# Optimization experiments

Hardware: AMD Instinct MI355X
Metric: run time of the kernel (lower is better)

## Reference

```python
import jax, jax.numpy as jnp
import numpy as np

V, D, H, HID, L, C, R, ALPHA = 32000, 768, 12, 3072, 2, 2, 8, 16
B, S = 64, 512
HD = D // H
SCALE = ALPHA / R

def _lin(x, W, b, A, Bm):
    # LoRA linear (eval mode, dropout=identity): x @ W^T + b + scaling * (x @ A^T) @ B^T
    return x @ W.T + b + (x @ A.T) @ Bm.T * SCALE

def _ln(x, g, b):
    m = x.mean(-1, keepdims=True)
    v = ((x - m) ** 2).mean(-1, keepdims=True)
    return (x - m) / jnp.sqrt(v + 1e-5) * g + b

def setup_inputs():
    ks = iter(jax.random.split(jax.random.key(0), 64))
    def nrm(shape):
        return jax.random.normal(next(ks), shape, dtype=jnp.float32) * 0.02
    inp = {"tokens": jax.random.randint(next(ks), (B, S), 0, V)}
    inp["emb_W"] = nrm((V, D)); inp["emb_A"] = nrm((R, V)); inp["emb_B"] = nrm((D, R))
    dims = {"q": (D, D), "k": (D, D), "v": (D, D), "o": (D, D), "1": (D, HID), "2": (HID, D)}
    for nm, (di, do) in dims.items():
        inp["W" + nm] = nrm((L, do, di)); inp["b" + nm] = jnp.zeros((L, do), jnp.float32)
        inp["A" + nm] = nrm((L, R, di)); inp["B" + nm] = nrm((L, do, R))
    inp["g1"] = jnp.ones((L, D), jnp.float32); inp["be1"] = jnp.zeros((L, D), jnp.float32)
    inp["g2"] = jnp.ones((L, D), jnp.float32); inp["be2"] = jnp.zeros((L, D), jnp.float32)
    inp["fcW"] = nrm((C, D)); inp["fcb"] = jnp.zeros((C,), jnp.float32)
    inp["fcA"] = nrm((R, D)); inp["fcB"] = nrm((C, R))
    return inp

def reference(tokens, emb_W, emb_A, emb_B,
              Wq, bq, Aq, Bq, Wk, bk, Ak, Bk, Wv, bv, Av, Bv, Wo, bo, Ao, Bo,
              W1, b1, A1, B1, W2, b2, A2, B2,
              g1, be1, g2, be2, fcW, fcb, fcA, fcB):
    # LoRA embedding: W[tok] + scaling * A^T[tok] @ B^T
    x = emb_W[tokens] + (emb_A.T[tokens] @ emb_B.T) * SCALE      # (B, S, D)
    x = jnp.transpose(x, (1, 0, 2))                              # (S, B, D)
    for l in range(L):
        Q = _lin(x, Wq[l], bq[l], Aq[l], Bq[l]).reshape(S, B, H, HD).transpose(0, 2, 1, 3)
        K = _lin(x, Wk[l], bk[l], Ak[l], Bk[l]).reshape(S, B, H, HD).transpose(0, 2, 1, 3)
        Vt = _lin(x, Wv[l], bv[l], Av[l], Bv[l]).reshape(S, B, H, HD).transpose(0, 2, 1, 3)
        # Faithful to the source: attention mixes over the BATCH axis (S, H, B, B)
        scores = jnp.einsum('shbd,shcd->shbc', Q, K) / jnp.sqrt(jnp.float32(HD))
        probs = jax.nn.softmax(scores, axis=-1)
        ao = jnp.einsum('shbc,shcd->shbd', probs, Vt).transpose(0, 2, 1, 3).reshape(S, B, D)
        ao = _lin(ao, Wo[l], bo[l], Ao[l], Bo[l])
        x = _ln(x + ao, g1[l], be1[l])
        ff = _lin(jax.nn.relu(_lin(x, W1[l], b1[l], A1[l], B1[l])), W2[l], b2[l], A2[l], B2[l])
        x = _ln(x + ff, g2[l], be2[l])
    return _lin(x.mean(0), fcW, fcb, fcA, fcB)                   # (B, C)
```

## Files before the change

kernel.cpp:

```cpp
#include <hip/hip_runtime.h>
#include <hip/hip_bf16.h>

#define VSZ   32000
#define DSZ   768
#define HN    12
#define HIDSZ 3072
#define NL    2
#define CN    2
#define RR    8
#define SCALEF 2.0f
#define BBATCH 64
#define SSEQ  512
#define HDIM  64
#define NTOK  (BBATCH*SSEQ)
#define QKVM  (3*DSZ)

typedef __attribute__((ext_vector_type(8))) short bf16x8;
typedef __attribute__((ext_vector_type(4))) float floatx4;

__device__ __forceinline__ unsigned short f2bf_raw(float f) {
    __hip_bfloat16 h = __float2bfloat16(f);
    return __builtin_bit_cast(unsigned short, h);
}
__device__ __forceinline__ float bf2f(__hip_bfloat16 h) {
    return __bfloat162float(h);
}

__device__ __forceinline__ void gload16(const void* g, void* l) {
    __builtin_amdgcn_global_load_lds(
        (const __attribute__((address_space(1))) unsigned int*)g,
        (__attribute__((address_space(3))) unsigned int*)l, 16, 0, 0);
}

__global__ __launch_bounds__(256) void embed_kernel(
    const int* __restrict__ tokens, const float* __restrict__ embW,
    const float* __restrict__ embA, const float* __restrict__ embB,
    __hip_bfloat16* __restrict__ xb)
{
    int n = blockIdx.x;
    int s = n / BBATCH, b = n % BBATCH;
    int tok = tokens[b * SSEQ + s];
    __shared__ float a[RR];
    if (threadIdx.x < RR) a[threadIdx.x] = embA[(size_t)threadIdx.x * VSZ + tok];
    __syncthreads();
    for (int d = threadIdx.x; d < DSZ; d += 256) {
        float val = embW[(size_t)tok * DSZ + d];
        float lo = 0.f;
        #pragma unroll
        for (int r = 0; r < RR; ++r) lo += a[r] * embB[d * RR + r];
        xb[(size_t)n * DSZ + d] = __float2bfloat16(val + SCALEF * lo);
    }
}

__global__ __launch_bounds__(256) void weff_kernel(
    const float* __restrict__ W, const float* __restrict__ A,
    const float* __restrict__ Bm, __hip_bfloat16* __restrict__ Weff, int K)
{
    int i = blockIdx.x * 256 + threadIdx.x;
    int o = blockIdx.y;
    float acc = W[(size_t)o * K + i];
    #pragma unroll
    for (int r = 0; r < RR; ++r)
        acc += SCALEF * Bm[o * RR + r] * A[(size_t)r * K + i];
    Weff[(size_t)o * K + i] = __float2bfloat16(acc);
}

__global__ __launch_bounds__(256) void biascat_kernel(
    const float* __restrict__ b0, const float* __restrict__ b1v,
    const float* __restrict__ b2v, float* __restrict__ out)
{
    int t = blockIdx.y * 256 + threadIdx.x;
    const float* src = (blockIdx.x == 0) ? b0 : (blockIdx.x == 1) ? b1v : b2v;
    out[blockIdx.x * DSZ + t] = src[t];
}

#define BM2  256
#define BK2  64
#define ABUF (BM2*BK2)

#define SB0() __builtin_amdgcn_sched_barrier(0)

__device__ __forceinline__ void stage_half(
    const unsigned short* __restrict__ g, unsigned short* l,
    int h, int ld, int k0, int t, int sk)
{
    #pragma unroll
    for (int it = 0; it < 2; ++it) {
        int rl = it * 64 + (t >> 3);
        gload16(g + (size_t)(h * 128 + rl) * ld + k0 + sk,
                l + (size_t)(h * 1024 + it * 512 + t) * 8);
    }
}

__device__ __forceinline__ void ph_exit() {
    __builtin_amdgcn_s_setprio(0);
    SB0();
    __builtin_amdgcn_s_barrier();
    SB0();
}

template<bool RELU, bool ADDRES>
__global__ __launch_bounds__(512, 2) void mgemm256_kernel(
    const __hip_bfloat16* __restrict__ X, const __hip_bfloat16* __restrict__ W,
    const float* __restrict__ bias, const __hip_bfloat16* __restrict__ res,
    __hip_bfloat16* __restrict__ Y, int K, int ldx, int ldy)
{
    __shared__ __align__(16) unsigned short As[2 * ABUF];
    __shared__ __align__(16) unsigned short Bs[2 * ABUF];

    const int t    = threadIdx.x;
    const int wv   = t >> 6;
    const int lane = t & 63;
    const int fm   = lane & 15;
    const int fq   = lane >> 4;
    const int wm   = wv >> 2;
    const int wn   = wv & 3;

    const int nbx = gridDim.x;
    const int nby = gridDim.y;
    int lin = blockIdx.y * nbx + blockIdx.x;
    {
        const int nwg = nbx * nby;
        int q = nwg >> 3, r = nwg & 7;
        int xcd = lin & 7, idx = lin >> 3;
        lin = (xcd < r ? xcd * (q + 1) : r * (q + 1) + (xcd - r) * q) + idx;
    }
    const int bn = lin % nby;
    const int bm = lin / nby;

    const unsigned short* Xg = (const unsigned short*)X + (size_t)bm * 256 * ldx;
    const unsigned short* Wg = (const unsigned short*)W + (size_t)bn * 256 * K;
    const int sk = ((t & 7) ^ ((t >> 3) & 7)) * 8;
    const int nt = K / BK2;

    floatx4 acc[2][2][4][2];
    #pragma unroll
    for (int a = 0; a < 2; ++a)
        #pragma unroll
        for (int b = 0; b < 2; ++b)
            #pragma unroll
            for (int c = 0; c < 4; ++c)
                #pragma unroll
                for (int d = 0; d < 2; ++d)
                    acc[a][b][c][d] = (floatx4){0.f, 0.f, 0.f, 0.f};

    const int swzg = (fq ^ (fm & 7)) * 8;
    int aoff[4], boff[2];
    #pragma unroll
    for (int mf = 0; mf < 4; ++mf) aoff[mf] = (wm * 64 + mf * 16 + fm) * 64 + swzg;
    #pragma unroll
    for (int nf = 0; nf < 2; ++nf) boff[nf] = (wn * 32 + nf * 16 + fm) * 64 + swzg;

    stage_half(Xg, As, 0, ldx, 0, t, sk);
    stage_half(Wg, Bs, 0, K,   0, t, sk);
    stage_half(Xg, As, 1, ldx, 0, t, sk);
    stage_half(Wg, Bs, 1, K,   0, t, sk);
    if (nt > 1) {
        stage_half(Xg, As + ABUF, 0, ldx, BK2, t, sk);
        stage_half(Wg, Bs + ABUF, 0, K,   BK2, t, sk);
        stage_half(Wg, Bs + ABUF, 1, K,   BK2, t, sk);
        asm volatile("s_waitcnt vmcnt(6)" ::: "memory");
    } else {
        asm volatile("s_waitcnt vmcnt(0)" ::: "memory");
    }
    SB0();
    __builtin_amdgcn_s_barrier();
    SB0();

    bf16x8 af0[4][2], af1[4][2], bf0[2][2], bf1[2][2];
    #pragma unroll
    for (int mf = 0; mf < 4; ++mf) {
        af0[mf][0] = *(const bf16x8*)&As[aoff[mf]];
        af0[mf][1] = *(const bf16x8*)&As[aoff[mf] ^ 32];
    }
    #pragma unroll
    for (int nf = 0; nf < 2; ++nf) {
        bf0[nf][0] = *(const bf16x8*)&Bs[boff[nf]];
        bf0[nf][1] = *(const bf16x8*)&Bs[boff[nf] ^ 32];
    }
    SB0();

    for (int kt = 0; kt < nt; ++kt) {
        const unsigned short* Ab = As + (kt & 1) * ABUF;
        const unsigned short* Bb = Bs + (kt & 1) * ABUF;
        unsigned short* AobW = As + ((kt & 1) ^ 1) * ABUF;
        const unsigned short* AobR = AobW;
        const unsigned short* BobR = Bs + ((kt & 1) ^ 1) * ABUF;
        unsigned short* Asame = (unsigned short*)Ab;
        unsigned short* Bsame = (unsigned short*)Bb;
        const int k1 = (kt + 1) * BK2;
        const int k2 = (kt + 2) * BK2;

        #pragma unroll
        for (int nf = 0; nf < 2; ++nf) {
            bf1[nf][0] = *(const bf16x8*)&Bb[(boff[nf] + 8192)];
            bf1[nf][1] = *(const bf16x8*)&Bb[(boff[nf] + 8192) ^ 32];
        }
        SB0();
        if (kt + 1 < nt) stage_half(Xg, AobW, 1, ldx, k1, t, sk);
        SB0();
        __builtin_amdgcn_s_barrier();
        asm volatile("s_waitcnt lgkmcnt(4)" ::: "memory");
        SB0();
        __builtin_amdgcn_s_setprio(1);
        #pragma unroll
        for (int mf = 0; mf < 4; ++mf)
            #pragma unroll
            for (int nf = 0; nf < 2; ++nf) {
                acc[0][0][mf][nf] = __builtin_amdgcn_mfma_f32_16x16x32_bf16(
                    af0[mf][0], bf0[nf][0], acc[0][0][mf][nf], 0, 0, 0);
                acc[0][0][mf][nf] = __builtin_amdgcn_mfma_f32_16x16x32_bf16(
                    af0[mf][1], bf0[nf][1], acc[0][0][mf][nf], 0, 0, 0);
            }
        ph_exit();

        #pragma unroll
        for (int mf = 0; mf < 4; ++mf) {
            af1[mf][0] = *(const bf16x8*)&Ab[(aoff[mf] + 8192)];
            af1[mf][1] = *(const bf16x8*)&Ab[(aoff[mf] + 8192) ^ 32];
        }
        SB0();
        if (kt + 2 < nt) stage_half(Xg, Asame, 0, ldx, k2, t, sk);
        SB0();
        __builtin_amdgcn_s_barrier();
        asm volatile("s_waitcnt lgkmcnt(8)" ::: "memory");
        SB0();
        __builtin_amdgcn_s_setprio(1);
        #pragma unroll
        for (int mf = 0; mf < 4; ++mf)
            #pragma unroll
            for (int nf = 0; nf < 2; ++nf) {
                acc[0][1][mf][nf] = __builtin_amdgcn_mfma_f32_16x16x32_bf16(
                    af0[mf][0], bf1[nf][0], acc[0][1][mf][nf], 0, 0, 0);
                acc[0][1][mf][nf] = __builtin_amdgcn_mfma_f32_16x16x32_bf16(
                    af0[mf][1], bf1[nf][1], acc[0][1][mf][nf], 0, 0, 0);
            }
        ph_exit();

        if (kt + 2 < nt) stage_half(Wg, Bsame, 0, K, k2, t, sk);
        SB0();
        __builtin_amdgcn_s_barrier();
        asm volatile("s_waitcnt lgkmcnt(0)" ::: "memory");
        SB0();
        __builtin_amdgcn_s_setprio(1);
        #pragma unroll
        for (int mf = 0; mf < 4; ++mf)
            #pragma unroll
            for (int nf = 0; nf < 2; ++nf) {
                acc[1][0][mf][nf] = __builtin_amdgcn_mfma_f32_16x16x32_bf16(
                    af1[mf][0], bf0[nf][0], acc[1][0][mf][nf], 0, 0, 0);
                acc[1][0][mf][nf] = __builtin_amdgcn_mfma_f32_16x16x32_bf16(
                    af1[mf][1], bf0[nf][1], acc[1][0][mf][nf], 0, 0, 0);
            }
        ph_exit();

        asm volatile("s_waitcnt vmcnt(4)" ::: "memory");
        SB0();
        if (kt + 1 < nt) {
            #pragma unroll
            for (int mf = 0; mf < 4; ++mf) {
                af0[mf][0] = *(const bf16x8*)&AobR[aoff[mf]];
                af0[mf][1] = *(const bf16x8*)&AobR[aoff[mf] ^ 32];
            }
            #pragma unroll
            for (int nf = 0; nf < 2; ++nf) {
                bf0[nf][0] = *(const bf16x8*)&BobR[boff[nf]];
                bf0[nf][1] = *(const bf16x8*)&BobR[boff[nf] ^ 32];
            }
        }
        SB0();
        if (kt + 2 < nt) stage_half(Wg, Bsame, 1, K, k2, t, sk);
        SB0();
        __builtin_amdgcn_s_barrier();
        SB0();
        __builtin_amdgcn_s_setprio(1);
        #pragma unroll
        for (int mf = 0; mf < 4; ++mf)
            #pragma unroll
            for (int nf = 0; nf < 2; ++nf) {
                acc[1][1][mf][nf] = __builtin_amdgcn_mfma_f32_16x16x32_bf16(
                    af1[mf][0], bf1[nf][0], acc[1][1][mf][nf], 0, 0, 0);
                acc[1][1][mf][nf] = __builtin_amdgcn_mfma_f32_16x16x32_bf16(
                    af1[mf][1], bf1[nf][1], acc[1][1][mf][nf], 0, 0, 0);
            }
        __builtin_amdgcn_s_setprio(0);
        SB0();
        if (kt + 2 < nt) {
            asm volatile("s_waitcnt vmcnt(6)" ::: "memory");
        } else if (kt + 1 < nt) {
            asm volatile("s_waitcnt vmcnt(0)" ::: "memory");
        }
        SB0();
        __builtin_amdgcn_s_barrier();
        SB0();
    }

    #pragma unroll
    for (int mh = 0; mh < 2; ++mh)
        #pragma unroll
        for (int nh = 0; nh < 2; ++nh)
            #pragma unroll
            for (int nf = 0; nf < 2; ++nf) {
                const int col = bn * 256 + nh * 128 + wn * 32 + nf * 16 + fm;
                const float bj = bias[col];
                #pragma unroll
                for (int mf = 0; mf < 4; ++mf) {
                    const int row0 = bm * 256 + mh * 128 + wm * 64 + mf * 16 + fq * 4;
                    #pragma unroll
                    for (int r = 0; r < 4; ++r) {
                        float v = acc[mh][nh][mf][nf][r] + bj;
                        if (RELU) v = fmaxf(v, 0.f);
                        size_t off = (size_t)(row0 + r) * ldy + col;
                        if (ADDRES) v += bf2f(res[off]);
                        Y[off] = __float2bfloat16(v);
                    }
                }
            }
}

__global__ __launch_bounds__(256) void attn_kernel(
    const __hip_bfloat16* __restrict__ qkvb, __hip_bfloat16* __restrict__ aob)
{
    __shared__ __align__(16) unsigned short Vt[64][72];
    __shared__ __align__(16) unsigned short Ps[4][16][72];
    const int t    = threadIdx.x;
    const int wv   = t >> 6;
    const int lane = t & 63;
    const int fm   = lane & 15;
    const int fq   = lane >> 4;
    const int sp   = blockIdx.x / HN;
    const int h    = blockIdx.x % HN;
    const unsigned short* qg =
        (const unsigned short*)qkvb + (size_t)sp * BBATCH * QKVM + h * HDIM;

    {
        const int c = lane, d0 = wv * 16;
        const unsigned short* vrow = qg + 2 * DSZ + (size_t)c * QKVM + d0;
        bf16x8 v0 = *(const bf16x8*)vrow;
        bf16x8 v1 = *(const bf16x8*)(vrow + 8);
        #pragma unroll
        for (int i = 0; i < 8; ++i) {
            Vt[d0 + i][c]     = (unsigned short)v0[i];
            Vt[d0 + 8 + i][c] = (unsigned short)v1[i];
        }
    }

    const unsigned short* qrow = qg + (size_t)(wv * 16 + fm) * QKVM + fq * 8;
    bf16x8 af0 = *(const bf16x8*)qrow;
    bf16x8 af1 = *(const bf16x8*)(qrow + 32);
    bf16x8 bk0[4], bk1[4];
    #pragma unroll
    for (int jt = 0; jt < 4; ++jt) {
        const unsigned short* krow = qg + DSZ + (size_t)(jt * 16 + fm) * QKVM + fq * 8;
        bk0[jt] = *(const bf16x8*)krow;
        bk1[jt] = *(const bf16x8*)(krow + 32);
    }

    floatx4 sc[4];
    #pragma unroll
    for (int jt = 0; jt < 4; ++jt) sc[jt] = (floatx4){0.f, 0.f, 0.f, 0.f};
    #pragma unroll
    for (int jt = 0; jt < 4; ++jt) {
        sc[jt] = __builtin_amdgcn_mfma_f32_16x16x32_bf16(af0, bk0[jt], sc[jt], 0, 0, 0);
        sc[jt] = __builtin_amdgcn_mfma_f32_16x16x32_bf16(af1, bk1[jt], sc[jt], 0, 0, 0);
    }
    #pragma unroll
    for (int jt = 0; jt < 4; ++jt)
        #pragma unroll
        for (int r = 0; r < 4; ++r) sc[jt][r] *= 0.125f;

    float pr[4][4];
    #pragma unroll
    for (int r = 0; r < 4; ++r) {
        float m = fmaxf(fmaxf(sc[0][r], sc[1][r]), fmaxf(sc[2][r], sc[3][r]));
        #pragma unroll
        for (int msk = 1; msk < 16; msk <<= 1) m = fmaxf(m, __shfl_xor(m, msk, 64));
        float s = 0.f;
        #pragma unroll
        for (int jt = 0; jt < 4; ++jt) { pr[jt][r] = __expf(sc[jt][r] - m); s += pr[jt][r]; }
        #pragma unroll
        for (int msk = 1; msk < 16; msk <<= 1) s += __shfl_xor(s, msk, 64);
        float inv = 1.f / s;
        #pragma unroll
        for (int jt = 0; jt < 4; ++jt) pr[jt][r] *= inv;
    }

    #pragma unroll
    for (int jt = 0; jt < 4; ++jt)
        #pragma unroll
        for (int r = 0; r < 4; ++r)
            Ps[wv][fq * 4 + r][jt * 16 + fm] = f2bf_raw(pr[jt][r]);

    __syncthreads();

    bf16x8 ap0 = *(const bf16x8*)&Ps[wv][fm][fq * 8];
    bf16x8 ap1 = *(const bf16x8*)&Ps[wv][fm][32 + fq * 8];
    floatx4 ov[4];
    #pragma unroll
    for (int jt = 0; jt < 4; ++jt) ov[jt] = (floatx4){0.f, 0.f, 0.f, 0.f};
    #pragma unroll
    for (int jt = 0; jt < 4; ++jt) {
        bf16x8 bv0 = *(const bf16x8*)&Vt[jt * 16 + fm][fq * 8];
        bf16x8 bv1 = *(const bf16x8*)&Vt[jt * 16 + fm][32 + fq * 8];
        ov[jt] = __builtin_amdgcn_mfma_f32_16x16x32_bf16(ap0, bv0, ov[jt], 0, 0, 0);
        ov[jt] = __builtin_amdgcn_mfma_f32_16x16x32_bf16(ap1, bv1, ov[jt], 0, 0, 0);
    }

    __hip_bfloat16* obase = aob + ((size_t)sp * BBATCH + wv * 16 + fq * 4) * DSZ + h * HDIM;
    #pragma unroll
    for (int jt = 0; jt < 4; ++jt)
        #pragma unroll
        for (int r = 0; r < 4; ++r)
            obase[(size_t)r * DSZ + jt * 16 + fm] = __float2bfloat16(ov[jt][r]);
}

__device__ __forceinline__ float block_sum256(float vsum, volatile float* red) {
    #pragma unroll
    for (int off = 32; off > 0; off >>= 1) vsum += __shfl_down(vsum, off, 64);
    if ((threadIdx.x & 63) == 0) red[threadIdx.x >> 6] = vsum;
    __syncthreads();
    return red[0] + red[1] + red[2] + red[3];
}

__global__ __launch_bounds__(256) void ln_kernel(
    const __hip_bfloat16* __restrict__ src, __hip_bfloat16* __restrict__ dst,
    const float* __restrict__ g, const float* __restrict__ be)
{
    __shared__ float red1[4];
    __shared__ float red2[4];
    const int n = blockIdx.x;
    const int t = threadIdx.x;
    const __hip_bfloat16* row = src + (size_t)n * DSZ;
    __hip_bfloat16* orow = dst + (size_t)n * DSZ;
    float v0 = bf2f(row[t]), v1 = bf2f(row[t + 256]), v2 = bf2f(row[t + 512]);
    float total = block_sum256(v0 + v1 + v2, red1);
    float mean = total * (1.0f / DSZ);
    float d0 = v0 - mean, d1 = v1 - mean, d2 = v2 - mean;
    __syncthreads();
    float var = block_sum256(d0 * d0 + d1 * d1 + d2 * d2, red2) * (1.0f / DSZ);
    float rstd = rsqrtf(var + 1e-5f);
    orow[t]       = __float2bfloat16(d0 * rstd * g[t]       + be[t]);
    orow[t + 256] = __float2bfloat16(d1 * rstd * g[t + 256] + be[t + 256]);
    orow[t + 512] = __float2bfloat16(d2 * rstd * g[t + 512] + be[t + 512]);
}

__global__ __launch_bounds__(256) void meanS_kernel(
    const __hip_bfloat16* __restrict__ x, float* __restrict__ xm)
{
    int idx = blockIdx.x * 256 + threadIdx.x;
    int b = idx / DSZ, d = idx % DSZ;
    float acc = 0.f;
    for (int s = 0; s < SSEQ; ++s)
        acc += bf2f(x[((size_t)s * BBATCH + b) * DSZ + d]);
    xm[idx] = acc * (1.0f / SSEQ);
}

__global__ __launch_bounds__(128) void fc_kernel(
    const float* __restrict__ xm, const float* __restrict__ fcW,
    const float* __restrict__ fcb, const float* __restrict__ fcA,
    const float* __restrict__ fcBm, float* __restrict__ out)
{
    int t = threadIdx.x;
    if (t >= BBATCH * CN) return;
    int b = t / CN, c = t % CN;
    float acc = fcb[c];
    float lora[RR];
    #pragma unroll
    for (int r = 0; r < RR; ++r) lora[r] = 0.f;
    for (int d = 0; d < DSZ; ++d) {
        float xv = xm[b * DSZ + d];
        acc += xv * fcW[c * DSZ + d];
        #pragma unroll
        for (int r = 0; r < RR; ++r) lora[r] += xv * fcA[r * DSZ + d];
    }
    float lo = 0.f;
    #pragma unroll
    for (int r = 0; r < RR; ++r) lo += lora[r] * fcBm[c * RR + r];
    out[b * CN + c] = acc + SCALEF * lo;
}

extern "C" void kernel_launch(void* const* d_in, const int* in_sizes, int n_in,
                              void* d_out, int out_size, void* d_ws, size_t ws_size,
                              hipStream_t stream) {
    const int*   tokens = (const int*)  d_in[0];
    const float* embW   = (const float*)d_in[1];
    const float* embA   = (const float*)d_in[2];
    const float* embB   = (const float*)d_in[3];
    const float* Wq = (const float*)d_in[4],  *bq = (const float*)d_in[5],
               * Aq = (const float*)d_in[6],  *Bq = (const float*)d_in[7];
    const float* Wk = (const float*)d_in[8],  *bk = (const float*)d_in[9],
               * Ak = (const float*)d_in[10], *Bk = (const float*)d_in[11];
    const float* Wv = (const float*)d_in[12], *bv = (const float*)d_in[13],
               * Av = (const float*)d_in[14], *Bv = (const float*)d_in[15];
    const float* Wo = (const float*)d_in[16], *bo = (const float*)d_in[17],
               * Ao = (const float*)d_in[18], *Bo = (const float*)d_in[19];
    const float* W1 = (const float*)d_in[20], *b1 = (const float*)d_in[21],
               * A1 = (const float*)d_in[22], *B1 = (const float*)d_in[23];
    const float* W2 = (const float*)d_in[24], *b2 = (const float*)d_in[25],
               * A2 = (const float*)d_in[26], *B2 = (const float*)d_in[27];
    const float* g1 = (const float*)d_in[28], *be1 = (const float*)d_in[29];
    const float* g2 = (const float*)d_in[30], *be2 = (const float*)d_in[31];
    const float* fcW = (const float*)d_in[32], *fcb = (const float*)d_in[33];
    const float* fcA = (const float*)d_in[34], *fcBm = (const float*)d_in[35];

    const size_t ND = (size_t)NTOK * DSZ;

    const size_t X_F    = ND / 2;
    const size_t XT_F   = ND / 2;
    const size_t WQKV_F = (size_t)QKVM * DSZ / 2;
    const size_t WO_F   = (size_t)DSZ * DSZ / 2;
    const size_t WF1_F  = (size_t)HIDSZ * DSZ / 2;
    const size_t WF2_F  = (size_t)DSZ * HIDSZ / 2;
    const size_t BQKV_F = 2304;
    const size_t XM_F   = (size_t)BBATCH * DSZ;
    const size_t fixedF = X_F + XT_F + WQKV_F + WO_F + WF1_F + WF2_F + BQKV_F + XM_F;
    const size_t availF = ws_size / 4;

    int schunk = 2;
    const int cand[6] = {512, 256, 128, 64, 32, 16};
    for (int i = 0; i < 6; ++i) {
        size_t chunkF = (size_t)cand[i] * BBATCH * (HIDSZ / 2);
        if (fixedF + chunkF <= availF) { schunk = cand[i]; break; }
    }
    const int Nc = schunk * BBATCH;
    const int nchunk = SSEQ / schunk;

    float* p = (float*)d_ws;
    __hip_bfloat16* x  = (__hip_bfloat16*)p;     p += X_F;
    __hip_bfloat16* xt = (__hip_bfloat16*)p;     p += XT_F;
    __hip_bfloat16* wqkvb = (__hip_bfloat16*)p;  p += WQKV_F;
    __hip_bfloat16* wob   = (__hip_bfloat16*)p;  p += WO_F;
    __hip_bfloat16* wf1b  = (__hip_bfloat16*)p;  p += WF1_F;
    __hip_bfloat16* wf2b  = (__hip_bfloat16*)p;  p += WF2_F;
    float* bqkv = p;                             p += BQKV_F;
    float* xm   = p;                             p += XM_F;
    __hip_bfloat16* cb16 = (__hip_bfloat16*)p;
    __hip_bfloat16* qkvb = cb16;
    __hip_bfloat16* aob  = cb16 + (size_t)Nc * QKVM;
    __hip_bfloat16* hb   = cb16;

    embed_kernel<<<NTOK, 256, 0, stream>>>(tokens, embW, embA, embB, x);

    for (int l = 0; l < NL; ++l) {
        const size_t oDD = (size_t)l * DSZ * DSZ;
        const size_t oDH = (size_t)l * HIDSZ * DSZ;
        const size_t oRD = (size_t)l * RR * DSZ;
        const size_t oRH = (size_t)l * RR * HIDSZ;
        const size_t oDR = (size_t)l * DSZ * RR;
        const size_t oHR = (size_t)l * HIDSZ * RR;

        weff_kernel<<<dim3(3, DSZ), 256, 0, stream>>>(Wq + oDD, Aq + oRD, Bq + oDR, wqkvb, DSZ);
        weff_kernel<<<dim3(3, DSZ), 256, 0, stream>>>(Wk + oDD, Ak + oRD, Bk + oDR, wqkvb + (size_t)DSZ * DSZ, DSZ);
        weff_kernel<<<dim3(3, DSZ), 256, 0, stream>>>(Wv + oDD, Av + oRD, Bv + oDR, wqkvb + (size_t)2 * DSZ * DSZ, DSZ);
        biascat_kernel<<<dim3(3, 3), 256, 0, stream>>>(bq + (size_t)l * DSZ, bk + (size_t)l * DSZ, bv + (size_t)l * DSZ, bqkv);
        weff_kernel<<<dim3(3, DSZ), 256, 0, stream>>>(Wo + oDD, Ao + oRD, Bo + oDR, wob, DSZ);
        weff_kernel<<<dim3(3, HIDSZ), 256, 0, stream>>>(W1 + oDH, A1 + oRD, B1 + oHR, wf1b, DSZ);
        weff_kernel<<<dim3(12, DSZ), 256, 0, stream>>>(W2 + oDH, A2 + oRH, B2 + oDR, wf2b, HIDSZ);

        const float* bo_l = bo + (size_t)l * DSZ;
        const float* b1_l = b1 + (size_t)l * HIDSZ;
        const float* b2_l = b2 + (size_t)l * DSZ;

        for (int c = 0; c < nchunk; ++c) {
            __hip_bfloat16* xc  = x  + (size_t)c * Nc * DSZ;
            __hip_bfloat16* xtc = xt + (size_t)c * Nc * DSZ;

            mgemm256_kernel<false, false><<<dim3(Nc / BM2, QKVM / BM2), 512, 0, stream>>>(
                xc, wqkvb, bqkv, nullptr, qkvb, DSZ, DSZ, QKVM);

            attn_kernel<<<schunk * HN, 256, 0, stream>>>(qkvb, aob);

            mgemm256_kernel<false, true><<<dim3(Nc / BM2, DSZ / BM2), 512, 0, stream>>>(
                aob, wob, bo_l, xc, xtc, DSZ, DSZ, DSZ);
            ln_kernel<<<Nc, 256, 0, stream>>>(xtc, xc, g1 + (size_t)l * DSZ, be1 + (size_t)l * DSZ);

            mgemm256_kernel<true, false><<<dim3(Nc / BM2, HIDSZ / BM2), 512, 0, stream>>>(
                xc, wf1b, b1_l, nullptr, hb, DSZ, DSZ, HIDSZ);

            mgemm256_kernel<false, true><<<dim3(Nc / BM2, DSZ / BM2), 512, 0, stream>>>(
                hb, wf2b, b2_l, xc, xtc, HIDSZ, HIDSZ, DSZ);
            ln_kernel<<<Nc, 256, 0, stream>>>(xtc, xc, g2 + (size_t)l * DSZ, be2 + (size_t)l * DSZ);
        }
    }

    meanS_kernel<<<(BBATCH * DSZ) / 256, 256, 0, stream>>>(x, xm);
    fc_kernel<<<1, 128, 0, stream>>>(xm, fcW, fcb, fcA, fcBm, (float*)d_out);
}
```

Before: 1.856 ms.

## Restructure GEMM LDS fragment loading and split FFN into row sub-chunks

The GEMM main loop no longer prefetches the next tile's A/B fragments during the last MFMA phase. Each phase now loads its fragments from the current buffer, waits with lgkmcnt(0), and places the barrier at phase exit, which simplifies the schedule but exposes more LDS latency. The templated kernel is split into four named kernel wrappers. The FFN1/FFN2 pair now runs on half-size row sub-chunks so the hidden activation buffer stays smaller and more cache-resident, at the cost of extra launches and smaller grids.

```diff
diff --git a/kernel.cpp b/kernel.cpp
--- a/kernel.cpp
+++ b/kernel.cpp
@@ -92,15 +92,8 @@
     }
 }
 
-__device__ __forceinline__ void ph_exit() {
-    __builtin_amdgcn_s_setprio(0);
-    SB0();
-    __builtin_amdgcn_s_barrier();
-    SB0();
-}
-
 template<bool RELU, bool ADDRES>
-__global__ __launch_bounds__(512, 2) void mgemm256_kernel(
+__device__ __forceinline__ void mgemm_body(
     const __hip_bfloat16* __restrict__ X, const __hip_bfloat16* __restrict__ W,
     const float* __restrict__ bias, const __hip_bfloat16* __restrict__ res,
     __hip_bfloat16* __restrict__ Y, int K, int ldx, int ldy)
@@ -167,40 +160,30 @@
     __builtin_amdgcn_s_barrier();
     SB0();
 
-    bf16x8 af0[4][2], af1[4][2], bf0[2][2], bf1[2][2];
-    #pragma unroll
-    for (int mf = 0; mf < 4; ++mf) {
-        af0[mf][0] = *(const bf16x8*)&As[aoff[mf]];
-        af0[mf][1] = *(const bf16x8*)&As[aoff[mf] ^ 32];
-    }
-    #pragma unroll
-    for (int nf = 0; nf < 2; ++nf) {
-        bf0[nf][0] = *(const bf16x8*)&Bs[boff[nf]];
-        bf0[nf][1] = *(const bf16x8*)&Bs[boff[nf] ^ 32];
-    }
-    SB0();
-
     for (int kt = 0; kt < nt; ++kt) {
         const unsigned short* Ab = As + (kt & 1) * ABUF;
         const unsigned short* Bb = Bs + (kt & 1) * ABUF;
-        unsigned short* AobW = As + ((kt & 1) ^ 1) * ABUF;
-        const unsigned short* AobR = AobW;
-        const unsigned short* BobR = Bs + ((kt & 1) ^ 1) * ABUF;
+        unsigned short* Aoth  = As + ((kt & 1) ^ 1) * ABUF;
         unsigned short* Asame = (unsigned short*)Ab;
         unsigned short* Bsame = (unsigned short*)Bb;
         const int k1 = (kt + 1) * BK2;
         const int k2 = (kt + 2) * BK2;
-
+        bf16x8 af0[4][2], af1[4][2], bf0[2][2], bf1[2][2];
+
+        #pragma unroll
+        for (int mf = 0; mf < 4; ++mf) {
+            af0[mf][0] = *(const bf16x8*)&Ab[aoff[mf]];
+            af0[mf][1] = *(const bf16x8*)&Ab[aoff[mf] ^ 32];
+        }
         #pragma unroll
         for (int nf = 0; nf < 2; ++nf) {
-            bf1[nf][0] = *(const bf16x8*)&Bb[(boff[nf] + 8192)];
-            bf1[nf][1] = *(const bf16x8*)&Bb[(boff[nf] + 8192) ^ 32];
-        }
-        SB0();
-        if (kt + 1 < nt) stage_half(Xg, AobW, 1, ldx, k1, t, sk);
-        SB0();
-        __builtin_amdgcn_s_barrier();
-        asm volatile("s_waitcnt lgkmcnt(4)" ::: "memory");
+            bf0[nf][0] = *(const bf16x8*)&Bb[boff[nf]];
+            bf0[nf][1] = *(const bf16x8*)&Bb[boff[nf] ^ 32];
+        }
+        SB0();
+        if (kt + 1 < nt) stage_half(Xg, Aoth, 1, ldx, k1, t, sk);
+        SB0();
+        asm volatile("s_waitcnt lgkmcnt(0)" ::: "memory");
         SB0();
         __builtin_amdgcn_s_setprio(1);
         #pragma unroll
@@ -212,18 +195,20 @@
                 acc[0][0][mf][nf] = __builtin_amdgcn_mfma_f32_16x16x32_bf16(
                     af0[mf][1], bf0[nf][1], acc[0][0][mf][nf], 0, 0, 0);
             }
-        ph_exit();
-
-        #pragma unroll
-        for (int mf = 0; mf < 4; ++mf) {
-            af1[mf][0] = *(const bf16x8*)&Ab[(aoff[mf] + 8192)];
-            af1[mf][1] = *(const bf16x8*)&Ab[(aoff[mf] + 8192) ^ 32];
+        __builtin_amdgcn_s_setprio(0);
+        SB0();
+        __builtin_amdgcn_s_barrier();
+        SB0();
+
+        #pragma unroll
+        for (int nf = 0; nf < 2; ++nf) {
+            bf1[nf][0] = *(const bf16x8*)&Bb[(boff[nf] + 8192)];
+            bf1[nf][1] = *(const bf16x8*)&Bb[(boff[nf] + 8192) ^ 32];
         }
         SB0();
         if (kt + 2 < nt) stage_half(Xg, Asame, 0, ldx, k2, t, sk);
         SB0();
-        __builtin_amdgcn_s_barrier();
-        asm volatile("s_waitcnt lgkmcnt(8)" ::: "memory");
+        asm volatile("s_waitcnt lgkmcnt(0)" ::: "memory");
         SB0();
         __builtin_amdgcn_s_setprio(1);
         #pragma unroll
@@ -235,11 +220,19 @@
                 acc[0][1][mf][nf] = __builtin_amdgcn_mfma_f32_16x16x32_bf16(
                     af0[mf][1], bf1[nf][1], acc[0][1][mf][nf], 0, 0, 0);
             }
-        ph_exit();
-
+        __builtin_amdgcn_s_setprio(0);
+        SB0();
+        __builtin_amdgcn_s_barrier();
+        SB0();
+
+        #pragma unroll
+        for (int mf = 0; mf < 4; ++mf) {
+            af1[mf][0] = *(const bf16x8*)&Ab[(aoff[mf] + 8192)];
+            af1[mf][1] = *(const bf16x8*)&Ab[(aoff[mf] + 8192) ^ 32];
+        }
+        SB0();
         if (kt + 2 < nt) stage_half(Wg, Bsame, 0, K, k2, t, sk);
         SB0();
-        __builtin_amdgcn_s_barrier();
         asm volatile("s_waitcnt lgkmcnt(0)" ::: "memory");
         SB0();
         __builtin_amdgcn_s_setprio(1);
@@ -252,26 +245,12 @@
                 acc[1][0][mf][nf] = __builtin_amdgcn_mfma_f32_16x16x32_bf16(
                     af1[mf][1], bf0[nf][1], acc[1][0][mf][nf], 0, 0, 0);
             }
-        ph_exit();
-
-        asm volatile("s_waitcnt vmcnt(4)" ::: "memory");
-        SB0();
-        if (kt + 1 < nt) {
-            #pragma unroll
-            for (int mf = 0; mf < 4; ++mf) {
-                af0[mf][0] = *(const bf16x8*)&AobR[aoff[mf]];
-                af0[mf][1] = *(const bf16x8*)&AobR[aoff[mf] ^ 32];
-            }
-            #pragma unroll
-            for (int nf = 0; nf < 2; ++nf) {
-                bf0[nf][0] = *(const bf16x8*)&BobR[boff[nf]];
-                bf0[nf][1] = *(const bf16x8*)&BobR[boff[nf] ^ 32];
-            }
-        }
-        SB0();
+        __builtin_amdgcn_s_setprio(0);
+        SB0();
+        __builtin_amdgcn_s_barrier();
+        SB0();
+
         if (kt + 2 < nt) stage_half(Wg, Bsame, 1, K, k2, t, sk);
-        SB0();
-        __builtin_amdgcn_s_barrier();
         SB0();
         __builtin_amdgcn_s_setprio(1);
         #pragma unroll
@@ -317,6 +296,30 @@
                 }
             }
 }
+
+__global__ __launch_bounds__(512, 2) void gemm_qkv(
+    const __hip_bfloat16* __restrict__ X, const __hip_bfloat16* __restrict__ W,
+    const float* __restrict__ bias, const __hip_bfloat16* __restrict__ res,
+    __hip_bfloat16* __restrict__ Y, int K, int ldx, int ldy)
+{ mgemm_body<false, false>(X, W, bias, res, Y, K, ldx, ldy); }
+
+__global__ __launch_bounds__(512, 2) void gemm_oproj(
+    const __hip_bfloat16* __restrict__ X, const __hip_bfloat16* __restrict__ W,
+    const float* __restrict__ bias, const __hip_bfloat16* __restrict__ res,
+    __hip_bfloat16* __restrict__ Y, int K, int ldx, int ldy)
+{ mgemm_body<false, true>(X, W, bias, res, Y, K, ldx, ldy); }
+
+__global__ __launch_bounds__(512, 2) void gemm_ff1(
+    const __hip_bfloat16* __restrict__ X, const __hip_bfloat16* __restrict__ W,
+    const float* __restrict__ bias, const __hip_bfloat16* __restrict__ res,
+    __hip_bfloat16* __restrict__ Y, int K, int ldx, int ldy)
+{ mgemm_body<true, false>(X, W, bias, res, Y, K, ldx, ldy); }
+
+__global__ __launch_bounds__(512, 2) void gemm_ff2(
+    const __hip_bfloat16* __restrict__ X, const __hip_bfloat16* __restrict__ W,
+    const float* __restrict__ bias, const __hip_bfloat16* __restrict__ res,
+    __hip_bfloat16* __restrict__ Y, int K, int ldx, int ldy)
+{ mgemm_body<false, true>(X, W, bias, res, Y, K, ldx, ldy); }
 
 __global__ __launch_bounds__(256) void attn_kernel(
     const __hip_bfloat16* __restrict__ qkvb, __hip_bfloat16* __restrict__ aob)
@@ -565,20 +568,24 @@
             __hip_bfloat16* xc  = x  + (size_t)c * Nc * DSZ;
             __hip_bfloat16* xtc = xt + (size_t)c * Nc * DSZ;
 
-            mgemm256_kernel<false, false><<<dim3(Nc / BM2, QKVM / BM2), 512, 0, stream>>>(
+            gemm_qkv<<<dim3(Nc / BM2, QKVM / BM2), 512, 0, stream>>>(
                 xc, wqkvb, bqkv, nullptr, qkvb, DSZ, DSZ, QKVM);
 
             attn_kernel<<<schunk * HN, 256, 0, stream>>>(qkvb, aob);
 
-            mgemm256_kernel<false, true><<<dim3(Nc / BM2, DSZ / BM2), 512, 0, stream>>>(
+            gemm_oproj<<<dim3(Nc / BM2, DSZ / BM2), 512, 0, stream>>>(
                 aob, wob, bo_l, xc, xtc, DSZ, DSZ, DSZ);
             ln_kernel<<<Nc, 256, 0, stream>>>(xtc, xc, g1 + (size_t)l * DSZ, be1 + (size_t)l * DSZ);
 
-            mgemm256_kernel<true, false><<<dim3(Nc / BM2, HIDSZ / BM2), 512, 0, stream>>>(
-                xc, wf1b, b1_l, nullptr, hb, DSZ, DSZ, HIDSZ);
-
-            mgemm256_kernel<false, true><<<dim3(Nc / BM2, DSZ / BM2), 512, 0, stream>>>(
-                hb, wf2b, b2_l, xc, xtc, HIDSZ, HIDSZ, DSZ);
+            const int nsub = (Nc >= 2 * BM2 && (Nc / 2) % BM2 == 0) ? 2 : 1;
+            const int Mh = Nc / nsub;
+            for (int sub = 0; sub < nsub; ++sub) {
+                const size_t soff = (size_t)sub * Mh * DSZ;
+                gemm_ff1<<<dim3(Mh / BM2, HIDSZ / BM2), 512, 0, stream>>>(
+                    xc + soff, wf1b, b1_l, nullptr, hb, DSZ, DSZ, HIDSZ);
+                gemm_ff2<<<dim3(Mh / BM2, DSZ / BM2), 512, 0, stream>>>(
+                    hb, wf2b, b2_l, xc + soff, xtc + soff, HIDSZ, HIDSZ, DSZ);
+            }
             ln_kernel<<<Nc, 256, 0, stream>>>(xtc, xc, g2 + (size_t)l * DSZ, be2 + (size_t)l * DSZ);
         }
     }
```

After: 1.740 ms. -6.2%, faster.
